# Kernel optimization log

Measured on AMD Instinct MI355X. Metric: run time of the kernel, lower is better.

The kernel has to match this reference:

```python
import jax, jax.numpy as jnp
import numpy as np

COS_EPS = 1e-6   # torch CosineSimilarity eps
NORM_EPS = 1e-10 # assignment-normalizer eps


def setup_inputs() -> dict:
    key = jax.random.key(0)
    ks = jax.random.split(key, 12)
    s = 0.1
    H, K, Din, Dout = 8, 128, 64, 64
    return {
        "node_set": jax.random.normal(ks[0], (32, Din, 1024, 12), jnp.float32),
        "adj": jax.random.uniform(ks[1], (32, 1024, 1024), jnp.float32),
        "W0": jax.random.normal(ks[2], (Din, Din), jnp.float32) * s,
        "w_i2c": jax.random.normal(ks[3], (H, 1), jnp.float32) * s,
        "b_i2c": jax.random.normal(ks[4], (H,), jnp.float32) * s,
        "W_lin": jax.random.normal(ks[5], (H * K, H), jnp.float32) * s,
        "b_lin": jax.random.normal(ks[6], (H * K,), jnp.float32) * s,
        "conv_w": jax.random.normal(ks[7], (H,), jnp.float32) * s,
        "conv_b": jax.random.normal(ks[8], (), jnp.float32) * s,
        "W_feat": jax.random.normal(ks[9], (Dout, Din), jnp.float32) * s,
        "b_feat": jax.random.normal(ks[10], (Dout,), jnp.float32) * s,
    }


def reference(node_set, adj, W0, w_i2c, b_i2c, W_lin, b_lin, conv_w, conv_b, W_feat, b_feat):
    # [B, C, N, T] -> [B, N, C, T] -> mean over T -> [B, N, D]
    x = jnp.mean(jnp.transpose(node_set, (0, 2, 1, 3)), axis=3)
    B = x.shape[0]
    H = w_i2c.shape[0]
    K = W_lin.shape[0] // H

    # get_att: attention-pooled global centroid seed [B, 1, D]
    temp = jnp.mean(x, axis=1, keepdims=True)                 # [B,1,D]
    h_avg = jnp.tanh(jnp.einsum('bod,de->boe', temp, W0))    # [B,1,D]
    att = jnp.einsum('bnd,bod->bno', x, h_avg)               # [B,N,1]
    cent = jnp.einsum('bno,bnd->bod', att, x)                # [B,1,D]

    # generate batch centroids: [B,D,1] -> [B,D,H] -> [B,D,H*K] -> [B,H,K,D]
    bc = jnp.transpose(cent, (0, 2, 1))                       # [B,D,1]
    bc = jax.nn.relu(bc @ w_i2c.T + b_i2c)                    # [B,D,H]
    bc = jax.nn.relu(bc @ W_lin.T + b_lin)                    # [B,D,H*K]
    bc = jnp.transpose(bc, (0, 2, 1)).reshape(B, H, K, -1)    # [B,H,K,D]

    # cosine-similarity assignment (no 5D repeat: dot / max(|x||c|, eps))
    dots = jnp.einsum('bnd,bhkd->bhkn', x, bc)                # [B,H,K,N]
    xn = jnp.linalg.norm(x, axis=-1)                          # [B,N]
    cn = jnp.linalg.norm(bc, axis=-1)                         # [B,H,K]
    C_heads = dots / jnp.maximum(cn[..., None] * xn[:, None, None, :], COS_EPS)
    # normalize over centroids dim (dim 2)
    C_heads = C_heads / (jnp.sum(C_heads, axis=2, keepdims=True) + NORM_EPS)

    # 1x1 conv over heads -> single assignment matrix [B,K,N]
    C = jnp.einsum('h,bhkn->bkn', conv_w, C_heads) + conv_b

    # pooled node features + output projection
    new_node_set = jnp.einsum('bkn,bnd->bkd', C, x)           # [B,K,D]
    return new_node_set @ W_feat.T + b_feat                   # [B,K,Dout]
```

## Files before the change

### kernel.cpp

```cpp
#include <hip/hip_runtime.h>
#include <math.h>

#define B_  32
#define N_  1024
#define D_  64
#define H_  8
#define K_  128
#define HK_ 1024

#define GLB(p) ((const __attribute__((address_space(1))) void*)(p))
#define LDSP(p) ((__attribute__((address_space(3))) void*)(p))

__global__ __launch_bounds__(512) void k1_mean(const float* __restrict__ ns,
        float* __restrict__ x, float* __restrict__ invxn,
        float* __restrict__ part1) {
    __shared__ float tile[64][65];
    int b    = blockIdx.x >> 4;
    int n0   = (blockIdx.x & 15) << 6;
    int lane = threadIdx.x & 63;
    int w    = threadIdx.x >> 6;
    #pragma unroll
    for (int j = 0; j < 8; ++j) {
        int d = w * 8 + j;
        const float4* p = (const float4*)(ns +
            ((size_t)((b * 64 + d) * 1024 + n0 + lane)) * 12);
        float4 a = p[0], c = p[1], e = p[2];
        float s = ((a.x + a.y) + (a.z + a.w)) + ((c.x + c.y) + (c.z + c.w))
                + ((e.x + e.y) + (e.z + e.w));
        tile[lane][d] = s * (1.0f / 12.0f);
    }
    __syncthreads();
    #pragma unroll
    for (int j = 0; j < 8; ++j) {
        int r = w * 8 + j;
        float v = tile[r][lane];
        x[((size_t)(b * 1024 + n0 + r)) * 64 + lane] = v;
        float ss = v * v;
        #pragma unroll
        for (int o = 32; o; o >>= 1) ss += __shfl_xor(ss, o);
        if (lane == 0) invxn[b * 1024 + n0 + r] = 1.0f / sqrtf(fmaxf(ss, 1e-30f));
    }
    if (threadIdx.x < 64) {
        float s = 0.0f;
        #pragma unroll 16
        for (int r = 0; r < 64; ++r) s += tile[r][threadIdx.x];
        part1[(size_t)blockIdx.x * 64 + threadIdx.x] = s;
    }
}

__global__ __launch_bounds__(256) void k3_cent(const float* __restrict__ x,
        const float* __restrict__ part1, const float* __restrict__ W0,
        float* __restrict__ part2) {
    __shared__ float t[64];
    __shared__ float ha[64];
    __shared__ float cp[4][64];
    int b    = blockIdx.x >> 3;
    int n0   = (blockIdx.x & 7) << 7;
    int lane = threadIdx.x & 63;
    int w    = threadIdx.x >> 6;
    if (threadIdx.x < 64) {
        float s = 0.0f;
        #pragma unroll
        for (int j = 0; j < 16; ++j) s += part1[(size_t)(b * 16 + j) * 64 + threadIdx.x];
        t[threadIdx.x] = s * (1.0f / 1024.0f);
    }
    __syncthreads();
    if (threadIdx.x < 64) {
        float a = 0.0f;
        #pragma unroll 8
        for (int d = 0; d < 64; ++d) a += t[d] * W0[d * 64 + threadIdx.x];
        ha[threadIdx.x] = tanhf(a);
    }
    __syncthreads();
    float hv = ha[lane];
    float cw = 0.0f;
    for (int nn = w; nn < 128; nn += 4) {
        float xv = x[((size_t)(b * 1024 + n0 + nn)) * 64 + lane];
        float d  = xv * hv;
        #pragma unroll
        for (int o = 32; o; o >>= 1) d += __shfl_xor(d, o);
        cw += d * xv;
    }
    cp[w][lane] = cw;
    __syncthreads();
    if (w == 0)
        part2[(size_t)blockIdx.x * 64 + lane] =
            ((cp[0][lane] + cp[1][lane]) + (cp[2][lane] + cp[3][lane]));
}

__global__ __launch_bounds__(256) void k4_bc(const float* __restrict__ part2,
        const float* __restrict__ w_i2c, const float* __restrict__ b_i2c,
        const float* __restrict__ W_lin, const float* __restrict__ b_lin,
        float* __restrict__ bc, float* __restrict__ invcn) {
    int lane = threadIdx.x & 63;
    int w    = threadIdx.x >> 6;
    int gg   = blockIdx.x * 4 + w;
    int b    = gg >> 8;
    int kk0  = (gg & 255) * 4;
    float c = 0.0f;
    #pragma unroll
    for (int s = 0; s < 8; ++s) c += part2[(size_t)(b * 8 + s) * 64 + lane];
    float b1[8];
    #pragma unroll
    for (int h = 0; h < 8; ++h) b1[h] = fmaxf(c * w_i2c[h] + b_i2c[h], 0.0f);
    #pragma unroll
    for (int u = 0; u < 4; ++u) {
        int kk = kk0 + u;
        float pre = b_lin[kk];
        #pragma unroll
        for (int h = 0; h < 8; ++h) pre += b1[h] * W_lin[kk * 8 + h];
        float v = fmaxf(pre, 0.0f);
        bc[((size_t)(b * 1024 + kk)) * 64 + lane] = v;
        float ss = v * v;
        #pragma unroll
        for (int o = 32; o; o >>= 1) ss += __shfl_xor(ss, o);
        if (lane == 0) invcn[b * 1024 + kk] = (ss > 0.0f) ? (1.0f / sqrtf(ss)) : 0.0f;
    }
}

__global__ __launch_bounds__(256, 1) void k5_assign(const float* __restrict__ x,
        const float* __restrict__ bc, const float* __restrict__ invxn,
        const float* __restrict__ invcn, const float* __restrict__ conv_w,
        const float* __restrict__ conv_b, float* __restrict__ C) {
    __shared__ float xt[128][68];
    __shared__ float bct[2][128 * 64];
    __shared__ float invx_s[128];
    __shared__ float invc_s[2][128];
    __shared__ float sredW[128][4];
    int b   = blockIdx.x >> 3;
    int n0  = (blockIdx.x & 7) << 7;
    int tid = threadIdx.x;
    int l   = tid & 63, w = tid >> 6;
    int q   = tid >> 4, p = tid & 15;
    int rxor = q & 7;
    int rl  = l >> 4, cl = l & 15;
    {
        int r = tid >> 1, dh = (tid & 1) << 5;
        const float4* src = (const float4*)(x + ((size_t)(b * 1024 + n0 + r)) * 64 + dh);
        float4* dst = (float4*)(&xt[r][dh]);
        #pragma unroll
        for (int u = 0; u < 8; ++u) dst[u] = src[u];
    }
    if (tid < 128) {
        invx_s[tid]    = invxn[b * 1024 + n0 + tid];
        invc_s[0][tid] = invcn[b * 1024 + tid];
    }
    {
        const float* hb = bc + ((size_t)(b * 1024)) * 64;
        #pragma unroll
        for (int t = 0; t < 8; ++t) {
            int chunk = w * 8 + t;
            int r = chunk * 4 + rl;
            const float* src = hb + (size_t)r * 64 + ((cl ^ (r & 7)) << 2);
            __builtin_amdgcn_global_load_lds(GLB(src), LDSP(&bct[0][chunk * 256]), 16, 0, 0);
        }
    }
    float Cacc[8][8];
    #pragma unroll
    for (int i = 0; i < 8; ++i)
        #pragma unroll
        for (int j = 0; j < 8; ++j) Cacc[i][j] = 0.0f;
    float cb = conv_b[0];
    __syncthreads();

    for (int h = 0; h < 8; ++h) {
        int cur = h & 1, nxt = cur ^ 1;
        float pfc = 0.0f;
        if (h < 7) {
            const float* hb = bc + ((size_t)(b * 1024 + (h + 1) * 128)) * 64;
            #pragma unroll
            for (int t = 0; t < 8; ++t) {
                int chunk = w * 8 + t;
                int r = chunk * 4 + rl;
                const float* src = hb + (size_t)r * 64 + ((cl ^ (r & 7)) << 2);
                __builtin_amdgcn_global_load_lds(GLB(src), LDSP(&bct[nxt][chunk * 256]), 16, 0, 0);
            }
            if (tid < 128) pfc = invcn[b * 1024 + (h + 1) * 128 + tid];
        }
        const float4* B4 = (const float4*)(&bct[cur][0]);
        float acc[8][8];
        #pragma unroll
        for (int i = 0; i < 8; ++i)
            #pragma unroll
            for (int j = 0; j < 8; ++j) acc[i][j] = 0.0f;
        float4 bvA[8], xvA[8], bvB[8], xvB[8];
        #pragma unroll
        for (int i = 0; i < 8; ++i) bvA[i] = B4[(q + 16 * i) * 16 + (0 ^ rxor)];
        #pragma unroll
        for (int j = 0; j < 8; ++j) xvA[j] = *(const float4*)(&xt[p + 16 * j][0]);
        #pragma unroll 1
        for (int c = 0; c < 16; c += 2) {
            #pragma unroll
            for (int i = 0; i < 8; ++i) bvB[i] = B4[(q + 16 * i) * 16 + ((c + 1) ^ rxor)];
            #pragma unroll
            for (int j = 0; j < 8; ++j) xvB[j] = *(const float4*)(&xt[p + 16 * j][(c + 1) << 2]);
            #pragma unroll
            for (int i = 0; i < 8; ++i)
                #pragma unroll
                for (int j = 0; j < 8; ++j)
                    acc[i][j] += bvA[i].x * xvA[j].x + bvA[i].y * xvA[j].y
                               + bvA[i].z * xvA[j].z + bvA[i].w * xvA[j].w;
            if (c + 2 < 16) {
                #pragma unroll
                for (int i = 0; i < 8; ++i) bvA[i] = B4[(q + 16 * i) * 16 + ((c + 2) ^ rxor)];
                #pragma unroll
                for (int j = 0; j < 8; ++j) xvA[j] = *(const float4*)(&xt[p + 16 * j][(c + 2) << 2]);
            }
            #pragma unroll
            for (int i = 0; i < 8; ++i)
                #pragma unroll
                for (int j = 0; j < 8; ++j)
                    acc[i][j] += bvB[i].x * xvB[j].x + bvB[i].y * xvB[j].y
                               + bvB[i].z * xvB[j].z + bvB[i].w * xvB[j].w;
        }
        float part[8];
        #pragma unroll
        for (int j = 0; j < 8; ++j) part[j] = 0.0f;
        #pragma unroll
        for (int i = 0; i < 8; ++i) {
            float ic = invc_s[cur][q + 16 * i];
            #pragma unroll
            for (int j = 0; j < 8; ++j) {
                float v = acc[i][j] * ic * invx_s[p + 16 * j];
                acc[i][j] = v;
                part[j] += v;
            }
        }
        #pragma unroll
        for (int j = 0; j < 8; ++j) {
            part[j] += __shfl_xor(part[j], 16);
            part[j] += __shfl_xor(part[j], 32);
        }
        if (l < 16) {
            #pragma unroll
            for (int j = 0; j < 8; ++j) sredW[p + 16 * j][w] = part[j];
        }
        __syncthreads();
        if (h < 7 && tid < 128) invc_s[nxt][tid] = pfc;
        float cwv = conv_w[h];
        #pragma unroll
        for (int j = 0; j < 8; ++j) {
            float4 sv = *(const float4*)(&sredW[p + 16 * j][0]);
            float s  = (sv.x + sv.y) + (sv.z + sv.w);
            float si = 1.0f / (s + 1e-10f);
            #pragma unroll
            for (int i = 0; i < 8; ++i) Cacc[i][j] += cwv * acc[i][j] * si;
        }
        __syncthreads();
    }
    #pragma unroll
    for (int i = 0; i < 8; ++i) {
        int k = q + 16 * i;
        #pragma unroll
        for (int j = 0; j < 8; ++j)
            C[((size_t)(b * 128 + k)) * 1024 + n0 + p + 16 * j] = Cacc[i][j] + cb;
    }
}

__global__ __launch_bounds__(256, 2) void k6_out(const float* __restrict__ C,
        const float* __restrict__ x, const float* __restrict__ Wf,
        const float* __restrict__ bfeat, float* __restrict__ out) {
    __shared__ float xt[128][68];
    __shared__ float ct[16][132];
    __shared__ float nnst[16][68];
    __shared__ float wfs[64][68];
    int b   = blockIdx.x >> 3;
    int k0  = (blockIdx.x & 7) << 4;
    int tid = threadIdx.x;
    int kq  = tid >> 4, p = tid & 15;
    for (int t = tid; t < 4096; t += 256) wfs[t >> 6][t & 63] = Wf[t];
    float acc[4] = {0.0f, 0.0f, 0.0f, 0.0f};
    for (int c = 0; c < 8; ++c) {
        __syncthreads();
        {
            int r = tid >> 1, dh = (tid & 1) << 5;
            const float4* src = (const float4*)(x + ((size_t)(b * 1024 + c * 128 + r)) * 64 + dh);
            float4* dst = (float4*)(&xt[r][dh]);
            #pragma unroll
            for (int u = 0; u < 8; ++u) dst[u] = src[u];
        }
        for (int t = tid; t < 2048; t += 256)
            ct[t >> 7][t & 127] = C[((size_t)(b * 128 + k0 + (t >> 7))) * 1024 + c * 128 + (t & 127)];
        __syncthreads();
        #pragma unroll 8
        for (int n = 0; n < 128; ++n) {
            float  cv = ct[kq][n];
            float4 xv = *(const float4*)(&xt[n][p << 2]);
            acc[0] += cv * xv.x; acc[1] += cv * xv.y;
            acc[2] += cv * xv.z; acc[3] += cv * xv.w;
        }
    }
    __syncthreads();
    nnst[kq][(p << 2) + 0] = acc[0];
    nnst[kq][(p << 2) + 1] = acc[1];
    nnst[kq][(p << 2) + 2] = acc[2];
    nnst[kq][(p << 2) + 3] = acc[3];
    __syncthreads();
    float o0 = bfeat[(p << 2) + 0], o1 = bfeat[(p << 2) + 1];
    float o2 = bfeat[(p << 2) + 2], o3 = bfeat[(p << 2) + 3];
    #pragma unroll
    for (int dc = 0; dc < 64; dc += 4) {
        float4 nv = *(const float4*)(&nnst[kq][dc]);
        float4 w0 = *(const float4*)(&wfs[(p << 2) + 0][dc]);
        float4 w1 = *(const float4*)(&wfs[(p << 2) + 1][dc]);
        float4 w2 = *(const float4*)(&wfs[(p << 2) + 2][dc]);
        float4 w3 = *(const float4*)(&wfs[(p << 2) + 3][dc]);
        o0 += nv.x * w0.x + nv.y * w0.y + nv.z * w0.z + nv.w * w0.w;
        o1 += nv.x * w1.x + nv.y * w1.y + nv.z * w1.z + nv.w * w1.w;
        o2 += nv.x * w2.x + nv.y * w2.y + nv.z * w2.z + nv.w * w2.w;
        o3 += nv.x * w3.x + nv.y * w3.y + nv.z * w3.z + nv.w * w3.w;
    }
    float4 ov = make_float4(o0, o1, o2, o3);
    *(float4*)(out + ((size_t)(b * 128 + k0 + kq)) * 64 + (p << 2)) = ov;
}

extern "C" void kernel_launch(void* const* d_in, const int* in_sizes, int n_in,
                              void* d_out, int out_size, void* d_ws, size_t ws_size,
                              hipStream_t stream) {
    const float* node_set = (const float*)d_in[0];
    const float* W0     = (const float*)d_in[2];
    const float* w_i2c  = (const float*)d_in[3];
    const float* b_i2c  = (const float*)d_in[4];
    const float* W_lin  = (const float*)d_in[5];
    const float* b_lin  = (const float*)d_in[6];
    const float* conv_w = (const float*)d_in[7];
    const float* conv_b = (const float*)d_in[8];
    const float* W_feat = (const float*)d_in[9];
    const float* b_feat = (const float*)d_in[10];
    float* out = (float*)d_out;
    float* ws  = (float*)d_ws;

    float* x     = ws;
    float* invxn = ws + 2097152;
    float* part1 = ws + 2129920;
    float* bc    = ws + 2162688;
    float* invcn = ws + 4259840;
    float* Cmat  = ws + 4292608;
    float* part2 = Cmat;

    k1_mean  <<<B_ * 16, 512, 0, stream>>>(node_set, x, invxn, part1);
    k3_cent  <<<B_ * 8,  256, 0, stream>>>(x, part1, W0, part2);
    k4_bc    <<<2048,    256, 0, stream>>>(part2, w_i2c, b_i2c, W_lin, b_lin, bc, invcn);
    k5_assign<<<B_ * 8,  256, 0, stream>>>(x, bc, invxn, invcn, conv_w, conv_b, Cmat);
    k6_out   <<<B_ * 8,  256, 0, stream>>>(Cmat, x, W_feat, b_feat, out);
}
```

Baseline: 396.0 us.

## Single-buffer centroid tile for 2 blocks/CU, batch-fastest block order, explicit FMA chains

k5_assign drops the double-buffered centroid LDS tile and raises launch bounds to two blocks per CU. The next head's tile is now loaded after the reduction barrier rather than prefetched during the matmul, so each block loses intra-block overlap and relies on the second resident block to hide that latency. Both k5 and k6 remap blockIdx so batch varies fastest, spreading concurrent blocks across batches. Dot products are rewritten as serial fmaf chains, and k6's inner loop now reads four C values per float4 load.

New measurement: 458.9 us. 1.16x slower.

```diff
diff --git a/kernel.cpp b/kernel.cpp
--- a/kernel.cpp
+++ b/kernel.cpp
@@ -118,17 +118,17 @@
     }
 }
 
-__global__ __launch_bounds__(256, 1) void k5_assign(const float* __restrict__ x,
+__global__ __launch_bounds__(256, 2) void k5_assign(const float* __restrict__ x,
         const float* __restrict__ bc, const float* __restrict__ invxn,
         const float* __restrict__ invcn, const float* __restrict__ conv_w,
         const float* __restrict__ conv_b, float* __restrict__ C) {
     __shared__ float xt[128][68];
-    __shared__ float bct[2][128 * 64];
+    __shared__ float bct[128 * 64];
     __shared__ float invx_s[128];
     __shared__ float invc_s[2][128];
     __shared__ float sredW[128][4];
-    int b   = blockIdx.x >> 3;
-    int n0  = (blockIdx.x & 7) << 7;
+    int b   = blockIdx.x & 31;
+    int n0  = (blockIdx.x >> 5) << 7;
     int tid = threadIdx.x;
     int l   = tid & 63, w = tid >> 6;
     int q   = tid >> 4, p = tid & 15;
@@ -152,7 +152,7 @@
             int chunk = w * 8 + t;
             int r = chunk * 4 + rl;
             const float* src = hb + (size_t)r * 64 + ((cl ^ (r & 7)) << 2);
-            __builtin_amdgcn_global_load_lds(GLB(src), LDSP(&bct[0][chunk * 256]), 16, 0, 0);
+            __builtin_amdgcn_global_load_lds(GLB(src), LDSP(&bct[chunk * 256]), 16, 0, 0);
         }
     }
     float Cacc[8][8];
@@ -161,23 +161,11 @@
         #pragma unroll
         for (int j = 0; j < 8; ++j) Cacc[i][j] = 0.0f;
     float cb = conv_b[0];
-    __syncthreads();
 
     for (int h = 0; h < 8; ++h) {
         int cur = h & 1, nxt = cur ^ 1;
-        float pfc = 0.0f;
-        if (h < 7) {
-            const float* hb = bc + ((size_t)(b * 1024 + (h + 1) * 128)) * 64;
-            #pragma unroll
-            for (int t = 0; t < 8; ++t) {
-                int chunk = w * 8 + t;
-                int r = chunk * 4 + rl;
-                const float* src = hb + (size_t)r * 64 + ((cl ^ (r & 7)) << 2);
-                __builtin_amdgcn_global_load_lds(GLB(src), LDSP(&bct[nxt][chunk * 256]), 16, 0, 0);
-            }
-            if (tid < 128) pfc = invcn[b * 1024 + (h + 1) * 128 + tid];
-        }
-        const float4* B4 = (const float4*)(&bct[cur][0]);
+        __syncthreads();
+        const float4* B4 = (const float4*)(&bct[0]);
         float acc[8][8];
         #pragma unroll
         for (int i = 0; i < 8; ++i)
@@ -198,8 +186,10 @@
             for (int i = 0; i < 8; ++i)
                 #pragma unroll
                 for (int j = 0; j < 8; ++j)
-                    acc[i][j] += bvA[i].x * xvA[j].x + bvA[i].y * xvA[j].y
-                               + bvA[i].z * xvA[j].z + bvA[i].w * xvA[j].w;
+                    acc[i][j] = fmaf(bvA[i].w, xvA[j].w,
+                                fmaf(bvA[i].z, xvA[j].z,
+                                fmaf(bvA[i].y, xvA[j].y,
+                                fmaf(bvA[i].x, xvA[j].x, acc[i][j]))));
             if (c + 2 < 16) {
                 #pragma unroll
                 for (int i = 0; i < 8; ++i) bvA[i] = B4[(q + 16 * i) * 16 + ((c + 2) ^ rxor)];
@@ -210,8 +200,10 @@
             for (int i = 0; i < 8; ++i)
                 #pragma unroll
                 for (int j = 0; j < 8; ++j)
-                    acc[i][j] += bvB[i].x * xvB[j].x + bvB[i].y * xvB[j].y
-                               + bvB[i].z * xvB[j].z + bvB[i].w * xvB[j].w;
+                    acc[i][j] = fmaf(bvB[i].w, xvB[j].w,
+                                fmaf(bvB[i].z, xvB[j].z,
+                                fmaf(bvB[i].y, xvB[j].y,
+                                fmaf(bvB[i].x, xvB[j].x, acc[i][j]))));
         }
         float part[8];
         #pragma unroll
@@ -236,7 +228,17 @@
             for (int j = 0; j < 8; ++j) sredW[p + 16 * j][w] = part[j];
         }
         __syncthreads();
-        if (h < 7 && tid < 128) invc_s[nxt][tid] = pfc;
+        if (h < 7) {
+            const float* hb = bc + ((size_t)(b * 1024 + (h + 1) * 128)) * 64;
+            #pragma unroll
+            for (int t = 0; t < 8; ++t) {
+                int chunk = w * 8 + t;
+                int r = chunk * 4 + rl;
+                const float* src = hb + (size_t)r * 64 + ((cl ^ (r & 7)) << 2);
+                __builtin_amdgcn_global_load_lds(GLB(src), LDSP(&bct[chunk * 256]), 16, 0, 0);
+            }
+            if (tid < 128) invc_s[nxt][tid] = invcn[b * 1024 + (h + 1) * 128 + tid];
+        }
         float cwv = conv_w[h];
         #pragma unroll
         for (int j = 0; j < 8; ++j) {
@@ -244,9 +246,8 @@
             float s  = (sv.x + sv.y) + (sv.z + sv.w);
             float si = 1.0f / (s + 1e-10f);
             #pragma unroll
-            for (int i = 0; i < 8; ++i) Cacc[i][j] += cwv * acc[i][j] * si;
-        }
-        __syncthreads();
+            for (int i = 0; i < 8; ++i) Cacc[i][j] = fmaf(cwv * si, acc[i][j], Cacc[i][j]);
+        }
     }
     #pragma unroll
     for (int i = 0; i < 8; ++i) {
@@ -264,12 +265,12 @@
     __shared__ float ct[16][132];
     __shared__ float nnst[16][68];
     __shared__ float wfs[64][68];
-    int b   = blockIdx.x >> 3;
-    int k0  = (blockIdx.x & 7) << 4;
+    int b   = blockIdx.x & 31;
+    int k0  = (blockIdx.x >> 5) << 4;
     int tid = threadIdx.x;
     int kq  = tid >> 4, p = tid & 15;
     for (int t = tid; t < 4096; t += 256) wfs[t >> 6][t & 63] = Wf[t];
-    float acc[4] = {0.0f, 0.0f, 0.0f, 0.0f};
+    float a0 = 0.0f, a1 = 0.0f, a2 = 0.0f, a3 = 0.0f;
     for (int c = 0; c < 8; ++c) {
         __syncthreads();
         {
@@ -282,19 +283,24 @@
         for (int t = tid; t < 2048; t += 256)
             ct[t >> 7][t & 127] = C[((size_t)(b * 128 + k0 + (t >> 7))) * 1024 + c * 128 + (t & 127)];
         __syncthreads();
-        #pragma unroll 8
-        for (int n = 0; n < 128; ++n) {
-            float  cv = ct[kq][n];
-            float4 xv = *(const float4*)(&xt[n][p << 2]);
-            acc[0] += cv * xv.x; acc[1] += cv * xv.y;
-            acc[2] += cv * xv.z; acc[3] += cv * xv.w;
-        }
-    }
-    __syncthreads();
-    nnst[kq][(p << 2) + 0] = acc[0];
-    nnst[kq][(p << 2) + 1] = acc[1];
-    nnst[kq][(p << 2) + 2] = acc[2];
-    nnst[kq][(p << 2) + 3] = acc[3];
+        #pragma unroll 4
+        for (int n = 0; n < 128; n += 4) {
+            float4 cv = *(const float4*)(&ct[kq][n]);
+            float4 x0 = *(const float4*)(&xt[n + 0][p << 2]);
+            float4 x1 = *(const float4*)(&xt[n + 1][p << 2]);
+            float4 x2 = *(const float4*)(&xt[n + 2][p << 2]);
+            float4 x3 = *(const float4*)(&xt[n + 3][p << 2]);
+            a0 = fmaf(cv.w, x3.x, fmaf(cv.z, x2.x, fmaf(cv.y, x1.x, fmaf(cv.x, x0.x, a0))));
+            a1 = fmaf(cv.w, x3.y, fmaf(cv.z, x2.y, fmaf(cv.y, x1.y, fmaf(cv.x, x0.y, a1))));
+            a2 = fmaf(cv.w, x3.z, fmaf(cv.z, x2.z, fmaf(cv.y, x1.z, fmaf(cv.x, x0.z, a2))));
+            a3 = fmaf(cv.w, x3.w, fmaf(cv.z, x2.w, fmaf(cv.y, x1.w, fmaf(cv.x, x0.w, a3))));
+        }
+    }
+    __syncthreads();
+    nnst[kq][(p << 2) + 0] = a0;
+    nnst[kq][(p << 2) + 1] = a1;
+    nnst[kq][(p << 2) + 2] = a2;
+    nnst[kq][(p << 2) + 3] = a3;
     __syncthreads();
     float o0 = bfeat[(p << 2) + 0], o1 = bfeat[(p << 2) + 1];
     float o2 = bfeat[(p << 2) + 2], o3 = bfeat[(p << 2) + 3];
@@ -305,10 +311,10 @@
         float4 w1 = *(const float4*)(&wfs[(p << 2) + 1][dc]);
         float4 w2 = *(const float4*)(&wfs[(p << 2) + 2][dc]);
         float4 w3 = *(const float4*)(&wfs[(p << 2) + 3][dc]);
-        o0 += nv.x * w0.x + nv.y * w0.y + nv.z * w0.z + nv.w * w0.w;
-        o1 += nv.x * w1.x + nv.y * w1.y + nv.z * w1.z + nv.w * w1.w;
-        o2 += nv.x * w2.x + nv.y * w2.y + nv.z * w2.z + nv.w * w2.w;
-        o3 += nv.x * w3.x + nv.y * w3.y + nv.z * w3.z + nv.w * w3.w;
+        o0 = fmaf(nv.w, w0.w, fmaf(nv.z, w0.z, fmaf(nv.y, w0.y, fmaf(nv.x, w0.x, o0))));
+        o1 = fmaf(nv.w, w1.w, fmaf(nv.z, w1.z, fmaf(nv.y, w1.y, fmaf(nv.x, w1.x, o1))));
+        o2 = fmaf(nv.w, w2.w, fmaf(nv.z, w2.z, fmaf(nv.y, w2.y, fmaf(nv.x, w2.x, o2))));
+        o3 = fmaf(nv.w, w3.w, fmaf(nv.z, w3.z, fmaf(nv.y, w3.y, fmaf(nv.x, w3.x, o3))));
     }
     float4 ov = make_float4(o0, o1, o2, o3);
     *(float4*)(out + ((size_t)(b * 128 + k0 + kq)) * 64 + (p << 2)) = ov;
```
